# Optimization experiments

Hardware: AMD Instinct MI355X
Metric: run time of the kernel (lower is better)

The kernel has to match this reference:

```python
import jax, jax.numpy as jnp
import numpy as np

B, L, D = 2, 2048, 2048
H, KVH, HD, FD = 8, 1, 256, 64   # heads, kv heads, head_dim, feature_dim
CHUNK = 64


def setup_inputs() -> dict:
    key = jax.random.key(0)
    ks = jax.random.split(key, 8)
    hidden_states = jax.random.normal(ks[0], (B, L, D), dtype=jnp.float32)
    # Gemma-style RoPE tables over half the head dim
    half = HD // 2
    inv_freq = 1.0 / (10000.0 ** (jnp.arange(half, dtype=jnp.float32) / half))
    ang = jnp.arange(L, dtype=jnp.float32)[:, None] * inv_freq[None, :]  # [L, half]
    freqs_cos, freqs_sin = jnp.cos(ang), jnp.sin(ang)
    mask = jnp.ones((1, 1, L, L), dtype=bool)  # unused in linear path
    s = 0.02
    Wq = jax.random.normal(ks[1], (D, H * HD), dtype=jnp.float32) * s
    Wk = jax.random.normal(ks[2], (D, KVH * HD), dtype=jnp.float32) * s
    Wv = jax.random.normal(ks[3], (D, KVH * HD), dtype=jnp.float32) * s
    Wo = jax.random.normal(ks[4], (H * HD, D), dtype=jnp.float32) * s
    fmq = jax.random.normal(ks[5], (H, HD, FD), dtype=jnp.float32) * s
    fmk = jax.random.normal(ks[6], (H, HD, FD), dtype=jnp.float32) * s
    return dict(hidden_states=hidden_states, freqs_cos=freqs_cos, freqs_sin=freqs_sin,
                mask=mask, Wq=Wq, Wk=Wk, Wv=Wv, Wo=Wo, fmq=fmq, fmk=fmk)


def _rope(x, cos, sin):
    # x: [B, L, h, HD]; Gemma complex RoPE: first half = real, second half = imag
    half = x.shape[-1] // 2
    x1, x2 = x[..., :half], x[..., half:]
    c = cos[None, :, None, :]
    s = sin[None, :, None, :]
    return jnp.concatenate([x1 * c - x2 * s, x1 * s + x2 * c], axis=-1)


def _hedgehog(x, W):
    # x: [B, H, L, HD], W: [H, HD, FD] -> softmax over cat([xW, -xW]) -> [B,H,L,2*FD]
    p = jnp.einsum('bhld,hdf->bhlf', x, W)
    return jax.nn.softmax(jnp.concatenate([p, -p], axis=-1), axis=-1)


def _chunk_linear_attn(q, k, v, chunk=CHUNK):
    # q,k: [B,H,L,F]; v: [B,H,L,HD]; chunked causal linear attention
    b, h, l, f = q.shape
    dv = v.shape[-1]
    n = l // chunk
    q = q.reshape(b, h, n, chunk, f) * (f ** -0.5)
    k = k.reshape(b, h, n, chunk, f)
    v = v.reshape(b, h, n, chunk, dv)
    kv = jnp.einsum('bhncf,bhncd->bhnfd', k, v)            # per-chunk KV
    kv = jnp.cumsum(kv, axis=2)
    kv = jnp.concatenate([jnp.zeros_like(kv[:, :, :1]), kv[:, :, :-1]], axis=2)  # exclusive prefix
    inter = jnp.einsum('bhncf,bhnfd->bhncd', q, kv)        # cross-chunk term
    s = jnp.einsum('bhnif,bhnjf->bhnij', q, k)             # intra-chunk scores
    tri = jnp.tril(jnp.ones((chunk, chunk), dtype=bool))
    s = jnp.where(tri, s, 0.0)
    intra = jnp.einsum('bhnij,bhnjd->bhnid', s, v)
    return (inter + intra).reshape(b, h, l, dv)


def reference(hidden_states, freqs_cos, freqs_sin, mask, Wq, Wk, Wv, Wo, fmq, fmk):
    b, l, _ = hidden_states.shape
    q = (hidden_states @ Wq).reshape(b, l, H, HD)
    k = (hidden_states @ Wk).reshape(b, l, KVH, HD)
    v = (hidden_states @ Wv).reshape(b, l, KVH, HD)
    q = _rope(q, freqs_cos, freqs_sin)
    k = _rope(k, freqs_cos, freqs_sin)
    # repeat_interleave kv heads to num_heads (MQA expansion)
    rep = H // KVH
    k = jnp.repeat(k, rep, axis=2)
    v = jnp.repeat(v, rep, axis=2)
    q = jnp.transpose(q, (0, 2, 1, 3))  # [B,H,L,HD]
    k = jnp.transpose(k, (0, 2, 1, 3))
    v = jnp.transpose(v, (0, 2, 1, 3))
    q = _hedgehog(q, fmq)
    k = _hedgehog(k, fmk)
    o = _chunk_linear_attn(q, k, v)                         # [B,H,L,HD]
    o = jnp.transpose(o, (0, 2, 1, 3)).reshape(b, l, H * HD)
    return o @ Wo
```

## Files before the change

### kernel.cpp

```cpp
#include <hip/hip_runtime.h>

#define B_ 2
#define L_ 2048
#define D_ 2048
#define H_ 8
#define HD_ 256
#define FD_ 64
#define F_ 128
#define NC_ 32
#define M_ (B_*L_)
#define SCALE_Q 0.08838834764831845f

typedef unsigned short u16;
typedef __attribute__((ext_vector_type(8))) short bf16x8;
typedef __attribute__((ext_vector_type(8))) unsigned short u16x8;
typedef __attribute__((ext_vector_type(16))) float f32x16;

#define FMA4(a_, s_, v_) { (a_).x += (s_)*(v_).x; (a_).y += (s_)*(v_).y; \
                           (a_).z += (s_)*(v_).z; (a_).w += (s_)*(v_).w; }


__device__ __forceinline__ u16 bf16_rne(float x) {
  unsigned u = __float_as_uint(x);
  return (u16)((u + 0x7fffu + ((u >> 16) & 1u)) >> 16);
}
__device__ __forceinline__ void bf16_split(float x, u16& h, u16& l) {
  unsigned u = __float_as_uint(x);
  unsigned hb = (u + 0x7fffu + ((u >> 16) & 1u)) >> 16;
  h = (u16)hb;
  float hf = __uint_as_float(hb << 16);
  l = bf16_rne(x - hf);
}

__device__ __forceinline__ void gl_lds16(const u16* g, u16* l) {
  __builtin_amdgcn_global_load_lds(
      (const __attribute__((address_space(1))) unsigned int*)g,
      (__attribute__((address_space(3))) unsigned int*)l, 16, 0, 0);
}

__device__ __forceinline__ void wtrans_body(const float* __restrict__ W, int Nsrc,
                                            int n0, u16* __restrict__ dst,
                                            int P, int kt) {
  int t = threadIdx.x;
  int nn = t & 127, kh = t >> 7;
  const float* src = W + (size_t)(kt * 32 + kh * 16) * Nsrc + n0 + nn;
  u16x8 u0, u1;
  #pragma unroll
  for (int kk = 0; kk < 8; ++kk) u0[kk] = bf16_rne(src[(size_t)kk * Nsrc]);
  #pragma unroll
  for (int kk = 0; kk < 8; ++kk) u1[kk] = bf16_rne(src[(size_t)(kk + 8) * Nsrc]);
  size_t base = ((size_t)P * 64 + kt) * 4096 + (size_t)((nn >> 6) & 1) * 2048
              + (size_t)kh * 1024 + (size_t)((nn >> 5) & 1) * 512
              + (size_t)(nn & 31) * 8;
  *(u16x8*)(dst + base) = u0;
  *(u16x8*)(dst + base + 256) = u1;
}

__global__ __launch_bounds__(256)
void prep_kernel(const float* __restrict__ hs,
                 const float* __restrict__ Wq, const float* __restrict__ Wk,
                 const float* __restrict__ Wv,
                 u16* __restrict__ hsHt, u16* __restrict__ hsLt,
                 u16* __restrict__ WTh) {
  int bid = blockIdx.x;
  if (bid < 4096) {
    int gid = bid * 256 + threadIdx.x;
    int r = gid >> 8, u = gid & 255;
    const float* src = hs + (size_t)r * 2048 + u * 8;
    float4 v0 = *(const float4*)src, v1 = *(const float4*)(src + 4);
    float vals[8] = {v0.x, v0.y, v0.z, v0.w, v1.x, v1.y, v1.z, v1.w};
    u16x8 hv, lv;
    #pragma unroll
    for (int j = 0; j < 8; ++j) { u16 hh, ll; bf16_split(vals[j], hh, ll); hv[j] = hh; lv[j] = ll; }
    size_t off = ((size_t)(r >> 6) * 64 + (u >> 2)) * 2048
               + (size_t)((u >> 1) & 1) * 1024 + (size_t)((r >> 5) & 1) * 512
               + (size_t)(u & 1) * 256 + (size_t)(r & 31) * 8;
    *(u16x8*)(hsHt + off) = hv;
    *(u16x8*)(hsLt + off) = lv;
  } else {
    int idx = bid - 4096;
    int P = idx >> 6, kt = idx & 63;
    const float* W; int Nsrc, n0;
    if (P < 16)      { W = Wq; Nsrc = 2048; n0 = P * 128; }
    else if (P < 18) { W = Wk; Nsrc = 256;  n0 = (P - 16) * 128; }
    else             { W = Wv; Nsrc = 256;  n0 = (P - 18) * 128; }
    wtrans_body(W, Nsrc, n0, WTh, P, kt);
  }
}

__global__ __launch_bounds__(256)
void wtrans_wo(const float* __restrict__ Wo, u16* __restrict__ WoTh) {
  wtrans_body(Wo, 2048, blockIdx.x * 128, WoTh, blockIdx.x, blockIdx.y);
}

__device__ __forceinline__ void mfma_body(
    const u16* __restrict__ AtH, const u16* __restrict__ AtL,
    const u16* __restrict__ Bt, float* __restrict__ C, int cstride,
    int bm, int bn) {
  __shared__ __align__(16) u16 AsH[2048];
  __shared__ __align__(16) u16 AsL[2048];
  __shared__ __align__(16) u16 Bs[4096];
  const int t = threadIdx.x, lane = t & 63, wv = t >> 6;
  const u16* aSrc = (wv ? AtL : AtH) + (size_t)bm * 131072 + lane * 8;
  const u16* bSrc = Bt + (size_t)bn * 262144 + wv * 2048 + lane * 8;
  u16* aDst = wv ? AsL : AsH;
  u16* bDst = Bs + wv * 2048;

  f32x16 acc[2][2];
  #pragma unroll
  for (int a = 0; a < 2; ++a)
    #pragma unroll
    for (int b2 = 0; b2 < 2; ++b2)
      #pragma unroll
      for (int r = 0; r < 16; ++r) acc[a][b2][r] = 0.f;

  for (int kt = 0; kt < 64; ++kt) {
    const u16* ak = aSrc + (size_t)kt * 2048;
    const u16* bk = bSrc + (size_t)kt * 4096;
    __syncthreads();
    #pragma unroll
    for (int c = 0; c < 4; ++c) {
      gl_lds16(ak + c * 512, aDst + c * 512);
      gl_lds16(bk + c * 512, bDst + c * 512);
    }
    __syncthreads();

    #pragma unroll
    for (int ks = 0; ks < 2; ++ks) {
      const u16* ph = AsH + ks * 1024 + lane * 8;
      const u16* pl = AsL + ks * 1024 + lane * 8;
      const u16* pb = Bs + wv * 2048 + ks * 1024 + lane * 8;
      bf16x8 a0 = *(const bf16x8*)ph;
      bf16x8 a1 = *(const bf16x8*)(ph + 512);
      bf16x8 b0 = *(const bf16x8*)pb;
      bf16x8 b1 = *(const bf16x8*)(pb + 512);
      acc[0][0] = __builtin_amdgcn_mfma_f32_32x32x16_bf16(a0, b0, acc[0][0], 0, 0, 0);
      acc[0][1] = __builtin_amdgcn_mfma_f32_32x32x16_bf16(a0, b1, acc[0][1], 0, 0, 0);
      acc[1][0] = __builtin_amdgcn_mfma_f32_32x32x16_bf16(a1, b0, acc[1][0], 0, 0, 0);
      acc[1][1] = __builtin_amdgcn_mfma_f32_32x32x16_bf16(a1, b1, acc[1][1], 0, 0, 0);
      bf16x8 l0 = *(const bf16x8*)pl;
      bf16x8 l1 = *(const bf16x8*)(pl + 512);
      acc[0][0] = __builtin_amdgcn_mfma_f32_32x32x16_bf16(l0, b0, acc[0][0], 0, 0, 0);
      acc[0][1] = __builtin_amdgcn_mfma_f32_32x32x16_bf16(l0, b1, acc[0][1], 0, 0, 0);
      acc[1][0] = __builtin_amdgcn_mfma_f32_32x32x16_bf16(l1, b0, acc[1][0], 0, 0, 0);
      acc[1][1] = __builtin_amdgcn_mfma_f32_32x32x16_bf16(l1, b1, acc[1][1], 0, 0, 0);
    }
  }

  const int fr = lane & 31, g = lane >> 5;
  float* Cp = C + (size_t)(bm * 64) * cstride + wv * 64;
  #pragma unroll
  for (int mt = 0; mt < 2; ++mt)
    #pragma unroll
    for (int nt = 0; nt < 2; ++nt) {
      #pragma unroll
      for (int r = 0; r < 16; ++r) {
        int row = mt * 32 + (r & 3) + 8 * (r >> 2) + 4 * g;
        Cp[(size_t)row * cstride + nt * 32 + fr] = acc[mt][nt][r];
      }
    }
}

#define SUB_ 20480

__device__ __forceinline__ void mfma_big_body(
    const u16* __restrict__ AtH, const u16* __restrict__ AtL,
    const u16* __restrict__ Bt, float* __restrict__ C, int cstride,
    int bm, int bn) {
  __shared__ __align__(16) u16 lds[3 * SUB_];
  const int t = threadIdx.x, lane = t & 63, wv = t >> 6;
  const int wm = wv >> 1, wn = wv & 1;

  const u16* gs[5];
  unsigned lo[5], gst[5];
  #pragma unroll
  for (int j = 0; j < 5; ++j) {
    int line = wv * 5 + j;
    if (line < 16) {
      gs[j] = AtH + ((size_t)(4 * bm + (line >> 2)) * 64) * 2048
                  + (size_t)(line & 3) * 512 + lane * 8;
      lo[j] = line * 512; gst[j] = 2048;
    } else if (line < 32) {
      int l2 = line - 16;
      gs[j] = AtL + ((size_t)(4 * bm + (l2 >> 2)) * 64) * 2048
                  + (size_t)(l2 & 3) * 512 + lane * 8;
      lo[j] = 8192 + l2 * 512; gst[j] = 2048;
    } else {
      int l3 = line - 32;
      gs[j] = Bt + (size_t)bn * 262144 + (size_t)l3 * 512 + lane * 8;
      lo[j] = 16384 + l3 * 512; gst[j] = 4096;
    }
  }

  f32x16 acc[2][2];
  #pragma unroll
  for (int a = 0; a < 2; ++a)
    #pragma unroll
    for (int b2 = 0; b2 < 2; ++b2)
      #pragma unroll
      for (int r = 0; r < 16; ++r) acc[a][b2][r] = 0.f;

  auto stage = [&](int kt_, int boff_) {
    #pragma unroll
    for (int j = 0; j < 5; ++j)
      gl_lds16(gs[j] + (size_t)kt_ * gst[j], lds + boff_ + lo[j]);
  };

  stage(0, 0);
  stage(1, SUB_);
  asm volatile("s_waitcnt vmcnt(5)" ::: "memory");
  __builtin_amdgcn_s_barrier();
  __builtin_amdgcn_sched_barrier(0);

  int cb = 0;
  for (int kt = 0; kt < 64; ++kt) {
    int sb = cb + 2 * SUB_; if (sb >= 3 * SUB_) sb -= 3 * SUB_;
    if (kt < 62) stage(kt + 2, sb);
    const u16* base = lds + cb;
    #pragma unroll
    for (int ks = 0; ks < 2; ++ks) {
      const u16* ph = base + wm * 2048 + ks * 1024 + lane * 8;
      const u16* pb = base + 16384 + wn * 2048 + ks * 1024 + lane * 8;
      bf16x8 a0 = *(const bf16x8*)ph;
      bf16x8 a1 = *(const bf16x8*)(ph + 512);
      bf16x8 l0 = *(const bf16x8*)(ph + 8192);
      bf16x8 l1 = *(const bf16x8*)(ph + 8704);
      bf16x8 b0 = *(const bf16x8*)pb;
      bf16x8 b1 = *(const bf16x8*)(pb + 512);
      __builtin_amdgcn_s_setprio(1);
      acc[0][0] = __builtin_amdgcn_mfma_f32_32x32x16_bf16(a0, b0, acc[0][0], 0, 0, 0);
      acc[0][1] = __builtin_amdgcn_mfma_f32_32x32x16_bf16(a0, b1, acc[0][1], 0, 0, 0);
      acc[1][0] = __builtin_amdgcn_mfma_f32_32x32x16_bf16(a1, b0, acc[1][0], 0, 0, 0);
      acc[1][1] = __builtin_amdgcn_mfma_f32_32x32x16_bf16(a1, b1, acc[1][1], 0, 0, 0);
      acc[0][0] = __builtin_amdgcn_mfma_f32_32x32x16_bf16(l0, b0, acc[0][0], 0, 0, 0);
      acc[0][1] = __builtin_amdgcn_mfma_f32_32x32x16_bf16(l0, b1, acc[0][1], 0, 0, 0);
      acc[1][0] = __builtin_amdgcn_mfma_f32_32x32x16_bf16(l1, b0, acc[1][0], 0, 0, 0);
      acc[1][1] = __builtin_amdgcn_mfma_f32_32x32x16_bf16(l1, b1, acc[1][1], 0, 0, 0);
      __builtin_amdgcn_s_setprio(0);
    }
    asm volatile("s_waitcnt lgkmcnt(0)" ::: "memory");
    if (kt < 62) asm volatile("s_waitcnt vmcnt(5)" ::: "memory");
    else         asm volatile("s_waitcnt vmcnt(0)" ::: "memory");
    __builtin_amdgcn_s_barrier();
    __builtin_amdgcn_sched_barrier(0);
    cb += SUB_; if (cb == 3 * SUB_) cb = 0;
  }

  const int fr = lane & 31, g = lane >> 5;
  float* Cp = C + (size_t)(bm * 256 + wm * 64) * cstride + wn * 64;
  #pragma unroll
  for (int mt = 0; mt < 2; ++mt)
    #pragma unroll
    for (int nt = 0; nt < 2; ++nt) {
      #pragma unroll
      for (int r = 0; r < 16; ++r) {
        int row = mt * 32 + (r & 3) + 8 * (r >> 2) + 4 * g;
        Cp[(size_t)row * cstride + nt * 32 + fr] = acc[mt][nt][r];
      }
    }
}

__global__ __launch_bounds__(512, 2)
void mfma_q(const u16* __restrict__ hsHt, const u16* __restrict__ hsLt,
            const u16* __restrict__ WTh, float* __restrict__ q) {
  mfma_big_body(hsHt, hsLt, WTh, q + blockIdx.x * 128, 2048,
                blockIdx.y, blockIdx.x);
}

__global__ __launch_bounds__(128, 4)
void mfma_kv(const u16* __restrict__ hsHt, const u16* __restrict__ hsLt,
             const u16* __restrict__ WTh,
             float* __restrict__ k, float* __restrict__ v) {
  int bn = blockIdx.x;
  float* Cb; int co;
  if (bn < 2) { Cb = k; co = bn * 128; }
  else        { Cb = v; co = (bn - 2) * 128; }
  mfma_body(hsHt, hsLt, WTh, Cb + co, 256, blockIdx.y, 16 + bn);
}

__global__ __launch_bounds__(512, 2)
void mfma_wo(const u16* __restrict__ oHt, const u16* __restrict__ oLt,
             const u16* __restrict__ WoTh, float* __restrict__ out) {
  mfma_big_body(oHt, oLt, WoTh, out + blockIdx.x * 128, 2048,
                blockIdx.y, blockIdx.x);
}

__device__ __forceinline__ float wave_max64(float v) {
  #pragma unroll
  for (int off = 32; off > 0; off >>= 1) v = fmaxf(v, __shfl_xor(v, off, 64));
  return v;
}
__device__ __forceinline__ float wave_sum64(float v) {
  #pragma unroll
  for (int off = 32; off > 0; off >>= 1) v += __shfl_xor(v, off, 64);
  return v;
}

__global__ __launch_bounds__(256)
void hedgehog_kernel(const float* __restrict__ q, const float* __restrict__ kx,
                     const float* __restrict__ fmq, const float* __restrict__ fmk,
                     const float* __restrict__ cosb, const float* __restrict__ sinb,
                     float* __restrict__ qf, float* __restrict__ kf) {
  __shared__ __align__(16) float rows[4][4][256];
  int bid = blockIdx.x;
  const float* x; const float* fm; float* out; int nh_in, gb;
  if (bid < 2048) { x = q;  fm = fmq; out = qf; nh_in = 8; gb = bid * 4; }
  else            { x = kx; fm = fmk; out = kf; nh_in = 1; gb = (bid - 2048) * 4; }
  int wave = threadIdx.x >> 6, lane = threadIdx.x & 63;
  int g = gb + wave;
  int l4 = g & (L_/4 - 1);
  int bh = g / (L_/4);
  int h = bh & 7, b = bh >> 3;
  int l0 = l4 * 4;
  size_t rstride = (nh_in == 1) ? (size_t)HD_ : (size_t)H_ * HD_;
  const float* xrow = (nh_in == 1)
      ? x + (size_t)(b * L_ + l0) * HD_
      : x + ((size_t)(b * L_ + l0) * H_ + h) * HD_;
  int dd = (lane & 31) * 4;
  #pragma unroll
  for (int r = 0; r < 4; ++r) {
    float4 v = *(const float4*)(xrow + r * rstride + lane * 4);
    float4 u;
    u.x = __shfl_xor(v.x, 32, 64); u.y = __shfl_xor(v.y, 32, 64);
    u.z = __shfl_xor(v.z, 32, 64); u.w = __shfl_xor(v.w, 32, 64);
    int l = l0 + r;
    float4 c = *(const float4*)(cosb + (size_t)l * 128 + dd);
    float4 s = *(const float4*)(sinb + (size_t)l * 128 + dd);
    float4 ro;
    if (lane < 32) {
      ro.x = v.x * c.x - u.x * s.x; ro.y = v.y * c.y - u.y * s.y;
      ro.z = v.z * c.z - u.z * s.z; ro.w = v.w * c.w - u.w * s.w;
    } else {
      ro.x = u.x * s.x + v.x * c.x; ro.y = u.y * s.y + v.y * c.y;
      ro.z = u.z * s.z + v.z * c.z; ro.w = u.w * s.w + v.w * c.w;
    }
    *(float4*)&rows[wave][r][lane * 4] = ro;
  }
  __syncthreads();

  const float* fmh = fm + (size_t)h * HD_ * FD_;
  float p0 = 0.f, p1 = 0.f, p2 = 0.f, p3 = 0.f;
  for (int d2 = 0; d2 < HD_; d2 += 4) {
    float w0 = fmh[(d2 + 0) * FD_ + lane];
    float w1 = fmh[(d2 + 1) * FD_ + lane];
    float w2 = fmh[(d2 + 2) * FD_ + lane];
    float w3 = fmh[(d2 + 3) * FD_ + lane];
    float4 r0 = *(const float4*)&rows[wave][0][d2];
    float4 r1 = *(const float4*)&rows[wave][1][d2];
    float4 r2 = *(const float4*)&rows[wave][2][d2];
    float4 r3 = *(const float4*)&rows[wave][3][d2];
    p0 += r0.x * w0 + r0.y * w1 + r0.z * w2 + r0.w * w3;
    p1 += r1.x * w0 + r1.y * w1 + r1.z * w2 + r1.w * w3;
    p2 += r2.x * w0 + r2.y * w1 + r2.z * w2 + r2.w * w3;
    p3 += r3.x * w0 + r3.y * w1 + r3.z * w2 + r3.w * w3;
  }
  float p[4] = {p0, p1, p2, p3};
  #pragma unroll
  for (int r = 0; r < 4; ++r) {
    float m = wave_max64(fabsf(p[r]));
    float e1 = __expf(p[r] - m);
    float e2 = __expf(-p[r] - m);
    float z = wave_sum64(e1 + e2);
    float inv = 1.0f / z;
    size_t base = ((size_t)bh * L_ + l0 + r) * F_;
    out[base + lane]      = e1 * inv;
    out[base + 64 + lane] = e2 * inv;
  }
}

__global__ __launch_bounds__(256)
void chunk_kv_kernel(const float* __restrict__ kf, const float* __restrict__ v,
                     float* __restrict__ kvc) {
  __shared__ __align__(16) float kfs[64][128];
  int n = blockIdx.x & (NC_ - 1), bh = blockIdx.x >> 5;
  int b = bh >> 3;
  const float* kfp = kf + ((size_t)bh * L_ + (size_t)n * 64) * F_;
  int t = threadIdx.x;
  #pragma unroll
  for (int it = 0; it < 8; ++it) {
    int flat = t * 4 + it * 1024;
    *(float4*)&kfs[flat >> 7][flat & 127] = *(const float4*)(kfp + flat);
  }
  __syncthreads();
  int dg = t & 63;
  int fg = t >> 6;
  const float* vp = v + (size_t)(b * L_ + n * 64) * HD_ + dg * 4;
  float* outp = kvc + (size_t)blockIdx.x * (F_ * HD_) + dg * 4;
  #pragma unroll
  for (int pass = 0; pass < 4; ++pass) {
    int f0 = fg * 8 + pass * 32;
    float4 acc[8];
    #pragma unroll
    for (int i = 0; i < 8; ++i) acc[i] = make_float4(0.f, 0.f, 0.f, 0.f);
    for (int j = 0; j < 64; ++j) {
      float4 vv = *(const float4*)(vp + (size_t)j * HD_);
      float4 ka = *(const float4*)&kfs[j][f0];
      float4 kb = *(const float4*)&kfs[j][f0 + 4];
      FMA4(acc[0], ka.x, vv); FMA4(acc[1], ka.y, vv);
      FMA4(acc[2], ka.z, vv); FMA4(acc[3], ka.w, vv);
      FMA4(acc[4], kb.x, vv); FMA4(acc[5], kb.y, vv);
      FMA4(acc[6], kb.z, vv); FMA4(acc[7], kb.w, vv);
    }
    #pragma unroll
    for (int ff = 0; ff < 8; ++ff)
      *(float4*)(outp + (size_t)(f0 + ff) * HD_) = acc[ff];
  }
}

__global__ __launch_bounds__(256)
void chunk_scan_kernel(float* __restrict__ kvc) {
  size_t gid = ((size_t)blockIdx.x * 256 + threadIdx.x) * 4;
  size_t bh = gid >> 15;
  size_t fd = gid & 32767;
  float* p = kvc + bh * ((size_t)NC_ * F_ * HD_) + fd;
  float4 run = make_float4(0.f, 0.f, 0.f, 0.f);
  #pragma unroll
  for (int n = 0; n < NC_; ++n) {
    float4 val = *(float4*)(p + (size_t)n * (F_ * HD_));
    *(float4*)(p + (size_t)n * (F_ * HD_)) = run;
    run.x += val.x; run.y += val.y; run.z += val.z; run.w += val.w;
  }
}

__global__ __launch_bounds__(256)
void chunk_attn_kernel(const float* __restrict__ qf, const float* __restrict__ kf,
                       const float* __restrict__ v, const float* __restrict__ kvc,
                       u16* __restrict__ oHt, u16* __restrict__ oLt) {
  __shared__ __align__(16) float qsT[128][68];
  __shared__ __align__(16) float ksS[128][68];
  float (*ssT)[68] = (float(*)[68])ksS;
  int n = blockIdx.x & (NC_ - 1), bh = blockIdx.x >> 5;
  int h = bh & 7, b = bh >> 3;
  int t = threadIdx.x;
  const float* qp = qf + ((size_t)bh * L_ + (size_t)n * 64) * F_;
  const float* kp = kf + ((size_t)bh * L_ + (size_t)n * 64) * F_;
  #pragma unroll
  for (int it = 0; it < 8; ++it) {
    int flat = t * 4 + it * 1024;
    int j = flat >> 7, f = flat & 127;
    float4 qv = *(const float4*)(qp + flat);
    qsT[f + 0][j] = qv.x * SCALE_Q; qsT[f + 1][j] = qv.y * SCALE_Q;
    qsT[f + 2][j] = qv.z * SCALE_Q; qsT[f + 3][j] = qv.w * SCALE_Q;
    float4 kv_ = *(const float4*)(kp + flat);
    ksS[f + 0][j] = kv_.x; ksS[f + 1][j] = kv_.y;
    ksS[f + 2][j] = kv_.z; ksS[f + 3][j] = kv_.w;
  }
  __syncthreads();

  float4 accs[4];
  {
    int j4 = (t & 15) * 4, i4 = (t >> 4) * 4;
    #pragma unroll
    for (int i = 0; i < 4; ++i) accs[i] = make_float4(0.f, 0.f, 0.f, 0.f);
    for (int f = 0; f < F_; ++f) {
      float4 a4 = *(const float4*)&qsT[f][i4];
      float4 b4 = *(const float4*)&ksS[f][j4];
      FMA4(accs[0], a4.x, b4); FMA4(accs[1], a4.y, b4);
      FMA4(accs[2], a4.z, b4); FMA4(accs[3], a4.w, b4);
    }
  }
  __syncthreads();
  {
    int j4 = (t & 15) * 4, i4 = (t >> 4) * 4;
    #pragma unroll
    for (int ii = 0; ii < 4; ++ii) {
      float sv[4] = {accs[ii].x, accs[ii].y, accs[ii].z, accs[ii].w};
      #pragma unroll
      for (int jj = 0; jj < 4; ++jj) {
        int i = i4 + ii, j = j4 + jj;
        ssT[j][i] = (j <= i) ? sv[jj] : 0.f;
      }
    }
  }
  __syncthreads();

  int dgrp = t & 31, rs = t >> 5;
  int d0 = dgrp * 8;
  int i0 = rs * 8;
  const float* kvp = kvc + (size_t)blockIdx.x * (F_ * HD_) + d0;
  const float* vp = v + (size_t)(b * L_ + n * 64) * HD_ + d0;
  float4 acc[8][2];
  #pragma unroll
  for (int i = 0; i < 8; ++i) {
    acc[i][0] = make_float4(0.f, 0.f, 0.f, 0.f);
    acc[i][1] = make_float4(0.f, 0.f, 0.f, 0.f);
  }
  for (int f = 0; f < F_; ++f) {
    float4 kv0 = *(const float4*)(kvp + (size_t)f * HD_);
    float4 kv1 = *(const float4*)(kvp + (size_t)f * HD_ + 4);
    float4 a0 = *(const float4*)&qsT[f][i0];
    float4 a1 = *(const float4*)&qsT[f][i0 + 4];
    FMA4(acc[0][0], a0.x, kv0); FMA4(acc[0][1], a0.x, kv1);
    FMA4(acc[1][0], a0.y, kv0); FMA4(acc[1][1], a0.y, kv1);
    FMA4(acc[2][0], a0.z, kv0); FMA4(acc[2][1], a0.z, kv1);
    FMA4(acc[3][0], a0.w, kv0); FMA4(acc[3][1], a0.w, kv1);
    FMA4(acc[4][0], a1.x, kv0); FMA4(acc[4][1], a1.x, kv1);
    FMA4(acc[5][0], a1.y, kv0); FMA4(acc[5][1], a1.y, kv1);
    FMA4(acc[6][0], a1.z, kv0); FMA4(acc[6][1], a1.z, kv1);
    FMA4(acc[7][0], a1.w, kv0); FMA4(acc[7][1], a1.w, kv1);
  }
  for (int j = 0; j < 64; ++j) {
    float4 v0 = *(const float4*)(vp + (size_t)j * HD_);
    float4 v1 = *(const float4*)(vp + (size_t)j * HD_ + 4);
    float4 s0 = *(const float4*)&ssT[j][i0];
    float4 s1 = *(const float4*)&ssT[j][i0 + 4];
    FMA4(acc[0][0], s0.x, v0); FMA4(acc[0][1], s0.x, v1);
    FMA4(acc[1][0], s0.y, v0); FMA4(acc[1][1], s0.y, v1);
    FMA4(acc[2][0], s0.z, v0); FMA4(acc[2][1], s0.z, v1);
    FMA4(acc[3][0], s0.w, v0); FMA4(acc[3][1], s0.w, v1);
    FMA4(acc[4][0], s1.x, v0); FMA4(acc[4][1], s1.x, v1);
    FMA4(acc[5][0], s1.y, v0); FMA4(acc[5][1], s1.y, v1);
    FMA4(acc[6][0], s1.z, v0); FMA4(acc[6][1], s1.z, v1);
    FMA4(acc[7][0], s1.w, v0); FMA4(acc[7][1], s1.w, v1);
  }
  int p = (b * L_ + n * 64) >> 6;
  size_t obase = ((size_t)p * 64 + h * 8 + (dgrp >> 2)) * 2048
               + (size_t)((dgrp >> 1) & 1) * 1024 + (size_t)(dgrp & 1) * 256;
  #pragma unroll
  for (int ii = 0; ii < 8; ++ii) {
    int i = i0 + ii;
    size_t off = obase + (size_t)((i >> 5) & 1) * 512 + (size_t)(i & 31) * 8;
    float vals[8] = {acc[ii][0].x, acc[ii][0].y, acc[ii][0].z, acc[ii][0].w,
                     acc[ii][1].x, acc[ii][1].y, acc[ii][1].z, acc[ii][1].w};
    u16x8 hv, lv;
    #pragma unroll
    for (int jj = 0; jj < 8; ++jj) { u16 hh, ll; bf16_split(vals[jj], hh, ll); hv[jj] = hh; lv[jj] = ll; }
    *(u16x8*)(oHt + off) = hv;
    *(u16x8*)(oLt + off) = lv;
  }
}

extern "C" void kernel_launch(void* const* d_in, const int* in_sizes, int n_in,
                              void* d_out, int out_size, void* d_ws, size_t ws_size,
                              hipStream_t stream) {
  const float* hs   = (const float*)d_in[0];
  const float* fcos = (const float*)d_in[1];
  const float* fsin = (const float*)d_in[2];
  const float* Wq  = (const float*)d_in[4];
  const float* Wk  = (const float*)d_in[5];
  const float* Wv  = (const float*)d_in[6];
  const float* Wo  = (const float*)d_in[7];
  const float* fmq = (const float*)d_in[8];
  const float* fmk = (const float*)d_in[9];
  float* out = (float*)d_out;

  float* ws = (float*)d_ws;
  float* q  = ws;
  float* k  = q  + (size_t)M_ * 2048;
  float* v  = k  + (size_t)M_ * 256;
  float* qf = v  + (size_t)M_ * 256;
  float* kf = qf + (size_t)B_ * H_ * L_ * F_;
  float* kv = kf + (size_t)B_ * H_ * L_ * F_;

  u16* hsHt = (u16*)kv;
  u16* hsLt = hsHt + (size_t)M_ * 2048;
  u16* WTh  = hsLt + (size_t)M_ * 2048;
  u16* WoTh = (u16*)kv;
  u16* oHt  = (u16*)q;
  u16* oLt  = oHt + (size_t)M_ * 2048;

  prep_kernel<<<4096 + 1280, 256, 0, stream>>>(hs, Wq, Wk, Wv, hsHt, hsLt, WTh);
  mfma_q<<<dim3(16, 16), 512, 0, stream>>>(hsHt, hsLt, WTh, q);
  mfma_kv<<<dim3(4, 64), 128, 0, stream>>>(hsHt, hsLt, WTh, k, v);
  hedgehog_kernel<<<2048 + 2048, 256, 0, stream>>>(q, k, fmq, fmk, fcos, fsin, qf, kf);
  chunk_kv_kernel<<<B_ * H_ * NC_, 256, 0, stream>>>(kf, v, kv);
  chunk_scan_kernel<<<(B_ * H_ * F_ * HD_) / 1024, 256, 0, stream>>>(kv);
  chunk_attn_kernel<<<B_ * H_ * NC_, 256, 0, stream>>>(qf, kf, v, kv, oHt, oLt);
  wtrans_wo<<<dim3(16, 64), 256, 0, stream>>>(Wo, WoTh);
  mfma_wo<<<dim3(16, 16), 512, 0, stream>>>(oHt, oLt, WoTh, out);
}
```

Before: 538.9 us.

## Move chunk attention onto bf16x3 MFMA with split-bf16 KV state layout

Rewrites the chunked linear-attention kernel to run the intra-chunk scores, masked S·V and Q·KV products on 32x32x16 bf16 MFMA. Each product uses a hi/lo bf16 split (three MFMAs) to keep close to fp32 accuracy. The per-chunk KV state is now stored directly as hi/lo bf16 in an MFMA-friendly tiled layout, and the scan runs on that format. The attention output is written as fp32 and converted by a separate prep_o pass before the output projection. This trades scalar FMA work for matrix-core throughput, at the cost of an extra output pass and repeated split/convert arithmetic.

```diff
diff --git a/kernel.cpp b/kernel.cpp
--- a/kernel.cpp
+++ b/kernel.cpp
@@ -15,6 +15,7 @@
 typedef __attribute__((ext_vector_type(8))) short bf16x8;
 typedef __attribute__((ext_vector_type(8))) unsigned short u16x8;
 typedef __attribute__((ext_vector_type(16))) float f32x16;
+typedef __attribute__((ext_vector_type(4))) unsigned int u32x4;
 
 #define FMA4(a_, s_, v_) { (a_).x += (s_)*(v_).x; (a_).y += (s_)*(v_).y; \
                            (a_).z += (s_)*(v_).z; (a_).w += (s_)*(v_).w; }
@@ -36,6 +37,13 @@
   __builtin_amdgcn_global_load_lds(
       (const __attribute__((address_space(1))) unsigned int*)g,
       (__attribute__((address_space(3))) unsigned int*)l, 16, 0, 0);
+}
+
+__device__ __forceinline__ size_t kvb_off(int d, int f) {
+  return (size_t)(((d >> 7) & 1) * 16384 + ((f >> 5) & 3) * 4096 +
+                  ((d >> 6) & 1) * 2048 + ((f >> 4) & 1) * 1024 +
+                  ((d >> 5) & 1) * 512 + ((f >> 3) & 1) * 256 +
+                  (d & 31) * 8 + (f & 7));
 }
 
 __device__ __forceinline__ void wtrans_body(const float* __restrict__ W, int Nsrc,
@@ -86,6 +94,24 @@
     else             { W = Wv; Nsrc = 256;  n0 = (P - 18) * 128; }
     wtrans_body(W, Nsrc, n0, WTh, P, kt);
   }
+}
+
+__global__ __launch_bounds__(256)
+void prep_o(const float* __restrict__ o, u16* __restrict__ oHt,
+            u16* __restrict__ oLt) {
+  int gid = blockIdx.x * 256 + threadIdx.x;
+  int r = gid >> 8, u = gid & 255;
+  const float* src = o + (size_t)r * 2048 + u * 8;
+  float4 v0 = *(const float4*)src, v1 = *(const float4*)(src + 4);
+  float vals[8] = {v0.x, v0.y, v0.z, v0.w, v1.x, v1.y, v1.z, v1.w};
+  u16x8 hv, lv;
+  #pragma unroll
+  for (int j = 0; j < 8; ++j) { u16 hh, ll; bf16_split(vals[j], hh, ll); hv[j] = hh; lv[j] = ll; }
+  size_t off = ((size_t)(r >> 6) * 64 + (u >> 2)) * 2048
+             + (size_t)((u >> 1) & 1) * 1024 + (size_t)((r >> 5) & 1) * 512
+             + (size_t)(u & 1) * 256 + (size_t)(r & 31) * 8;
+  *(u16x8*)(oHt + off) = hv;
+  *(u16x8*)(oLt + off) = lv;
 }
 
 __global__ __launch_bounds__(256)
@@ -370,7 +396,7 @@
 
 __global__ __launch_bounds__(256)
 void chunk_kv_kernel(const float* __restrict__ kf, const float* __restrict__ v,
-                     float* __restrict__ kvc) {
+                     u16* __restrict__ kvbH, u16* __restrict__ kvbL) {
   __shared__ __align__(16) float kfs[64][128];
   int n = blockIdx.x & (NC_ - 1), bh = blockIdx.x >> 5;
   int b = bh >> 3;
@@ -385,7 +411,7 @@
   int dg = t & 63;
   int fg = t >> 6;
   const float* vp = v + (size_t)(b * L_ + n * 64) * HD_ + dg * 4;
-  float* outp = kvc + (size_t)blockIdx.x * (F_ * HD_) + dg * 4;
+  size_t cb = (size_t)blockIdx.x * 32768;
   #pragma unroll
   for (int pass = 0; pass < 4; ++pass) {
     int f0 = fg * 8 + pass * 32;
@@ -402,132 +428,228 @@
       FMA4(acc[6], kb.z, vv); FMA4(acc[7], kb.w, vv);
     }
     #pragma unroll
-    for (int ff = 0; ff < 8; ++ff)
-      *(float4*)(outp + (size_t)(f0 + ff) * HD_) = acc[ff];
+    for (int c = 0; c < 4; ++c) {
+      u16x8 hv, lv;
+      #pragma unroll
+      for (int ff = 0; ff < 8; ++ff) {
+        float xs = (c == 0) ? acc[ff].x : (c == 1) ? acc[ff].y
+                 : (c == 2) ? acc[ff].z : acc[ff].w;
+        u16 hh, ll; bf16_split(xs, hh, ll); hv[ff] = hh; lv[ff] = ll;
+      }
+      int d = dg * 4 + c;
+      size_t off = cb + kvb_off(d, f0);
+      *(u16x8*)(kvbH + off) = hv;
+      *(u16x8*)(kvbL + off) = lv;
+    }
   }
 }
 
 __global__ __launch_bounds__(256)
-void chunk_scan_kernel(float* __restrict__ kvc) {
-  size_t gid = ((size_t)blockIdx.x * 256 + threadIdx.x) * 4;
-  size_t bh = gid >> 15;
-  size_t fd = gid & 32767;
-  float* p = kvc + bh * ((size_t)NC_ * F_ * HD_) + fd;
-  float4 run = make_float4(0.f, 0.f, 0.f, 0.f);
-  #pragma unroll
+void chunk_scan_kernel(u16* __restrict__ kvbH, u16* __restrict__ kvbL) {
+  int bh = blockIdx.x >> 4, g = blockIdx.x & 15;
+  int d = threadIdx.x;
+  size_t off = kvb_off(d, g * 8);
+  float run[8] = {0.f, 0.f, 0.f, 0.f, 0.f, 0.f, 0.f, 0.f};
   for (int n = 0; n < NC_; ++n) {
-    float4 val = *(float4*)(p + (size_t)n * (F_ * HD_));
-    *(float4*)(p + (size_t)n * (F_ * HD_)) = run;
-    run.x += val.x; run.y += val.y; run.z += val.z; run.w += val.w;
-  }
-}
-
-__global__ __launch_bounds__(256)
+    size_t a = ((size_t)(bh * 32 + n)) * 32768 + off;
+    u16x8 hv = *(u16x8*)(kvbH + a);
+    u16x8 lv = *(u16x8*)(kvbL + a);
+    u16x8 oh, ol;
+    #pragma unroll
+    for (int c = 0; c < 8; ++c) {
+      float val = __uint_as_float((unsigned)hv[c] << 16)
+                + __uint_as_float((unsigned)lv[c] << 16);
+      u16 hh, ll; bf16_split(run[c], hh, ll); oh[c] = hh; ol[c] = ll;
+      run[c] += val;
+    }
+    *(u16x8*)(kvbH + a) = oh;
+    *(u16x8*)(kvbL + a) = ol;
+  }
+}
+
+#define MFB(a_, b_, c_) (c_) = __builtin_amdgcn_mfma_f32_32x32x16_bf16((a_), (b_), (c_), 0, 0, 0)
+
+__global__ __launch_bounds__(256, 2)
 void chunk_attn_kernel(const float* __restrict__ qf, const float* __restrict__ kf,
-                       const float* __restrict__ v, const float* __restrict__ kvc,
-                       u16* __restrict__ oHt, u16* __restrict__ oLt) {
-  __shared__ __align__(16) float qsT[128][68];
-  __shared__ __align__(16) float ksS[128][68];
-  float (*ssT)[68] = (float(*)[68])ksS;
-  int n = blockIdx.x & (NC_ - 1), bh = blockIdx.x >> 5;
-  int h = bh & 7, b = bh >> 3;
-  int t = threadIdx.x;
-  const float* qp = qf + ((size_t)bh * L_ + (size_t)n * 64) * F_;
-  const float* kp = kf + ((size_t)bh * L_ + (size_t)n * 64) * F_;
-  #pragma unroll
-  for (int it = 0; it < 8; ++it) {
-    int flat = t * 4 + it * 1024;
-    int j = flat >> 7, f = flat & 127;
-    float4 qv = *(const float4*)(qp + flat);
-    qsT[f + 0][j] = qv.x * SCALE_Q; qsT[f + 1][j] = qv.y * SCALE_Q;
-    qsT[f + 2][j] = qv.z * SCALE_Q; qsT[f + 3][j] = qv.w * SCALE_Q;
-    float4 kv_ = *(const float4*)(kp + flat);
-    ksS[f + 0][j] = kv_.x; ksS[f + 1][j] = kv_.y;
-    ksS[f + 2][j] = kv_.z; ksS[f + 3][j] = kv_.w;
+                       const float* __restrict__ v,
+                       const u16* __restrict__ kvbH, const u16* __restrict__ kvbL,
+                       float* __restrict__ o) {
+  __shared__ __align__(16) u16 lds[32768];
+  const int n = blockIdx.x & (NC_ - 1), bh = blockIdx.x >> 5;
+  const int h = bh & 7, b = bh >> 3;
+  const int t = threadIdx.x;
+  const int w = t >> 6, i31 = t & 31, G = (t >> 5) & 1;
+  const int l8 = (t & 63) * 8;
+
+  {
+    const float* qp = qf + ((size_t)bh * L_ + (size_t)n * 64) * F_;
+    const float* kp = kf + ((size_t)bh * L_ + (size_t)n * 64) * F_;
+    int o8 = t & 15, ib = t >> 4;
+    #pragma unroll
+    for (int iter = 0; iter < 4; ++iter) {
+      int i = ib + iter * 16;
+      int it = i >> 5, ks = o8 >> 1;
+      int sub = (it * 8 + ks) * 512 + (o8 & 1) * 256 + (i & 31) * 8;
+      {
+        const float* src = qp + (size_t)i * 128 + o8 * 8;
+        float4 a = *(const float4*)src, c = *(const float4*)(src + 4);
+        float vals[8] = {a.x, a.y, a.z, a.w, c.x, c.y, c.z, c.w};
+        u16x8 hv, lv;
+        #pragma unroll
+        for (int j = 0; j < 8; ++j) {
+          u16 hh, ll; bf16_split(vals[j] * SCALE_Q, hh, ll);
+          hv[j] = hh; lv[j] = ll;
+        }
+        *(u16x8*)(lds + sub) = hv;
+        *(u16x8*)(lds + 8192 + sub) = lv;
+      }
+      {
+        const float* src = kp + (size_t)i * 128 + o8 * 8;
+        float4 a = *(const float4*)src, c = *(const float4*)(src + 4);
+        float vals[8] = {a.x, a.y, a.z, a.w, c.x, c.y, c.z, c.w};
+        u16x8 hv, lv;
+        #pragma unroll
+        for (int j = 0; j < 8; ++j) {
+          u16 hh, ll; bf16_split(vals[j], hh, ll);
+          hv[j] = hh; lv[j] = ll;
+        }
+        *(u16x8*)(lds + 16384 + sub) = hv;
+        *(u16x8*)(lds + 24576 + sub) = lv;
+      }
+    }
   }
   __syncthreads();
 
-  float4 accs[4];
+  const u16* Lq  = lds;
+  const u16* Lql = lds + 8192;
+  const u16* Lk  = lds + 16384;
+  const u16* Lkl = lds + 24576;
+
+  f32x16 st[2][2];
+  #pragma unroll
+  for (int a = 0; a < 2; ++a)
+    #pragma unroll
+    for (int c = 0; c < 2; ++c)
+      #pragma unroll
+      for (int r = 0; r < 16; ++r) st[a][c][r] = 0.f;
+
+  #pragma unroll
+  for (int ks = 0; ks < 8; ++ks) {
+    bf16x8 kh0 = *(const bf16x8*)(Lk  + ks * 512 + l8);
+    bf16x8 kh1 = *(const bf16x8*)(Lk  + (8 + ks) * 512 + l8);
+    bf16x8 kl0 = *(const bf16x8*)(Lkl + ks * 512 + l8);
+    bf16x8 kl1 = *(const bf16x8*)(Lkl + (8 + ks) * 512 + l8);
+    bf16x8 qh0 = *(const bf16x8*)(Lq  + ks * 512 + l8);
+    bf16x8 qh1 = *(const bf16x8*)(Lq  + (8 + ks) * 512 + l8);
+    bf16x8 ql0 = *(const bf16x8*)(Lql + ks * 512 + l8);
+    bf16x8 ql1 = *(const bf16x8*)(Lql + (8 + ks) * 512 + l8);
+    MFB(kh0, qh0, st[0][0]); MFB(kh0, ql0, st[0][0]); MFB(kl0, qh0, st[0][0]);
+    MFB(kh0, qh1, st[0][1]); MFB(kh0, ql1, st[0][1]); MFB(kl0, qh1, st[0][1]);
+    MFB(kh1, qh0, st[1][0]); MFB(kh1, ql0, st[1][0]); MFB(kl1, qh0, st[1][0]);
+    MFB(kh1, qh1, st[1][1]); MFB(kh1, ql1, st[1][1]); MFB(kl1, qh1, st[1][1]);
+  }
+
+  bf16x8 sfH[2][4], sfL[2][4];
+  #pragma unroll
+  for (int mt = 0; mt < 2; ++mt) {
+    int iv = mt * 32 + i31;
+    #pragma unroll
+    for (int ksj = 0; ksj < 4; ++ksj) {
+      const int jt = ksj >> 1, kb = ksj & 1;
+      unsigned ph[4], pl[4];
+      #pragma unroll
+      for (int half = 0; half < 2; ++half) {
+        u16 hh[4], ll[4];
+        #pragma unroll
+        for (int c = 0; c < 4; ++c) {
+          int r = 8 * kb + 4 * half + c;
+          int jv = jt * 32 + (r & 3) + 8 * (r >> 2) + 4 * G;
+          float mv = (jv <= iv) ? st[jt][mt][r] : 0.f;
+          u16 h_, l_; bf16_split(mv, h_, l_);
+          hh[c] = h_; ll[c] = l_;
+        }
+        ph[half * 2 + 0] = (unsigned)hh[0] | ((unsigned)hh[1] << 16);
+        ph[half * 2 + 1] = (unsigned)hh[2] | ((unsigned)hh[3] << 16);
+        pl[half * 2 + 0] = (unsigned)ll[0] | ((unsigned)ll[1] << 16);
+        pl[half * 2 + 1] = (unsigned)ll[2] | ((unsigned)ll[3] << 16);
+      }
+      unsigned rH1 = (unsigned)__shfl_xor((int)(G ? ph[0] : ph[2]), 32, 64);
+      unsigned rH2 = (unsigned)__shfl_xor((int)(G ? ph[1] : ph[3]), 32, 64);
+      unsigned rL1 = (unsigned)__shfl_xor((int)(G ? pl[0] : pl[2]), 32, 64);
+      unsigned rL2 = (unsigned)__shfl_xor((int)(G ? pl[1] : pl[3]), 32, 64);
+      u32x4 wH, wL;
+      wH[0] = G ? rH1 : ph[0]; wH[1] = G ? rH2 : ph[1];
+      wH[2] = G ? ph[2] : rH1; wH[3] = G ? ph[3] : rH2;
+      wL[0] = G ? rL1 : pl[0]; wL[1] = G ? rL2 : pl[1];
+      wL[2] = G ? pl[2] : rL1; wL[3] = G ? pl[3] : rL2;
+      sfH[mt][ksj] = __builtin_bit_cast(bf16x8, wH);
+      sfL[mt][ksj] = __builtin_bit_cast(bf16x8, wL);
+    }
+  }
+
+  f32x16 acc[2][2];
+  #pragma unroll
+  for (int a = 0; a < 2; ++a)
+    #pragma unroll
+    for (int c = 0; c < 2; ++c)
+      #pragma unroll
+      for (int r = 0; r < 16; ++r) acc[a][c][r] = 0.f;
+
   {
-    int j4 = (t & 15) * 4, i4 = (t >> 4) * 4;
-    #pragma unroll
-    for (int i = 0; i < 4; ++i) accs[i] = make_float4(0.f, 0.f, 0.f, 0.f);
-    for (int f = 0; f < F_; ++f) {
-      float4 a4 = *(const float4*)&qsT[f][i4];
-      float4 b4 = *(const float4*)&ksS[f][j4];
-      FMA4(accs[0], a4.x, b4); FMA4(accs[1], a4.y, b4);
-      FMA4(accs[2], a4.z, b4); FMA4(accs[3], a4.w, b4);
-    }
-  }
-  __syncthreads();
+    const float* vp = v + (size_t)(b * L_ + n * 64) * HD_;
+    #pragma unroll
+    for (int nt = 0; nt < 2; ++nt) {
+      #pragma unroll
+      for (int ksj = 0; ksj < 4; ++ksj) {
+        const float* vsrc = vp + (size_t)(ksj * 16 + G * 8) * HD_
+                          + w * 64 + nt * 32 + i31;
+        u16x8 vh, vl;
+        #pragma unroll
+        for (int c = 0; c < 8; ++c) {
+          u16 hh, ll; bf16_split(vsrc[(size_t)c * HD_], hh, ll);
+          vh[c] = hh; vl[c] = ll;
+        }
+        bf16x8 vH = __builtin_bit_cast(bf16x8, vh);
+        bf16x8 vL = __builtin_bit_cast(bf16x8, vl);
+        MFB(sfH[0][ksj], vH, acc[0][nt]); MFB(sfL[0][ksj], vH, acc[0][nt]);
+        MFB(sfH[0][ksj], vL, acc[0][nt]);
+        MFB(sfH[1][ksj], vH, acc[1][nt]); MFB(sfL[1][ksj], vH, acc[1][nt]);
+        MFB(sfH[1][ksj], vL, acc[1][nt]);
+      }
+    }
+  }
+
   {
-    int j4 = (t & 15) * 4, i4 = (t >> 4) * 4;
-    #pragma unroll
-    for (int ii = 0; ii < 4; ++ii) {
-      float sv[4] = {accs[ii].x, accs[ii].y, accs[ii].z, accs[ii].w};
-      #pragma unroll
-      for (int jj = 0; jj < 4; ++jj) {
-        int i = i4 + ii, j = j4 + jj;
-        ssT[j][i] = (j <= i) ? sv[jj] : 0.f;
-      }
-    }
-  }
-  __syncthreads();
-
-  int dgrp = t & 31, rs = t >> 5;
-  int d0 = dgrp * 8;
-  int i0 = rs * 8;
-  const float* kvp = kvc + (size_t)blockIdx.x * (F_ * HD_) + d0;
-  const float* vp = v + (size_t)(b * L_ + n * 64) * HD_ + d0;
-  float4 acc[8][2];
-  #pragma unroll
-  for (int i = 0; i < 8; ++i) {
-    acc[i][0] = make_float4(0.f, 0.f, 0.f, 0.f);
-    acc[i][1] = make_float4(0.f, 0.f, 0.f, 0.f);
-  }
-  for (int f = 0; f < F_; ++f) {
-    float4 kv0 = *(const float4*)(kvp + (size_t)f * HD_);
-    float4 kv1 = *(const float4*)(kvp + (size_t)f * HD_ + 4);
-    float4 a0 = *(const float4*)&qsT[f][i0];
-    float4 a1 = *(const float4*)&qsT[f][i0 + 4];
-    FMA4(acc[0][0], a0.x, kv0); FMA4(acc[0][1], a0.x, kv1);
-    FMA4(acc[1][0], a0.y, kv0); FMA4(acc[1][1], a0.y, kv1);
-    FMA4(acc[2][0], a0.z, kv0); FMA4(acc[2][1], a0.z, kv1);
-    FMA4(acc[3][0], a0.w, kv0); FMA4(acc[3][1], a0.w, kv1);
-    FMA4(acc[4][0], a1.x, kv0); FMA4(acc[4][1], a1.x, kv1);
-    FMA4(acc[5][0], a1.y, kv0); FMA4(acc[5][1], a1.y, kv1);
-    FMA4(acc[6][0], a1.z, kv0); FMA4(acc[6][1], a1.z, kv1);
-    FMA4(acc[7][0], a1.w, kv0); FMA4(acc[7][1], a1.w, kv1);
-  }
-  for (int j = 0; j < 64; ++j) {
-    float4 v0 = *(const float4*)(vp + (size_t)j * HD_);
-    float4 v1 = *(const float4*)(vp + (size_t)j * HD_ + 4);
-    float4 s0 = *(const float4*)&ssT[j][i0];
-    float4 s1 = *(const float4*)&ssT[j][i0 + 4];
-    FMA4(acc[0][0], s0.x, v0); FMA4(acc[0][1], s0.x, v1);
-    FMA4(acc[1][0], s0.y, v0); FMA4(acc[1][1], s0.y, v1);
-    FMA4(acc[2][0], s0.z, v0); FMA4(acc[2][1], s0.z, v1);
-    FMA4(acc[3][0], s0.w, v0); FMA4(acc[3][1], s0.w, v1);
-    FMA4(acc[4][0], s1.x, v0); FMA4(acc[4][1], s1.x, v1);
-    FMA4(acc[5][0], s1.y, v0); FMA4(acc[5][1], s1.y, v1);
-    FMA4(acc[6][0], s1.z, v0); FMA4(acc[6][1], s1.z, v1);
-    FMA4(acc[7][0], s1.w, v0); FMA4(acc[7][1], s1.w, v1);
-  }
-  int p = (b * L_ + n * 64) >> 6;
-  size_t obase = ((size_t)p * 64 + h * 8 + (dgrp >> 2)) * 2048
-               + (size_t)((dgrp >> 1) & 1) * 1024 + (size_t)(dgrp & 1) * 256;
-  #pragma unroll
-  for (int ii = 0; ii < 8; ++ii) {
-    int i = i0 + ii;
-    size_t off = obase + (size_t)((i >> 5) & 1) * 512 + (size_t)(i & 31) * 8;
-    float vals[8] = {acc[ii][0].x, acc[ii][0].y, acc[ii][0].z, acc[ii][0].w,
-                     acc[ii][1].x, acc[ii][1].y, acc[ii][1].z, acc[ii][1].w};
-    u16x8 hv, lv;
-    #pragma unroll
-    for (int jj = 0; jj < 8; ++jj) { u16 hh, ll; bf16_split(vals[jj], hh, ll); hv[jj] = hh; lv[jj] = ll; }
-    *(u16x8*)(oHt + off) = hv;
-    *(u16x8*)(oLt + off) = lv;
-  }
+    size_t cb = (size_t)blockIdx.x * 32768;
+    #pragma unroll
+    for (int ks = 0; ks < 8; ++ks) {
+      bf16x8 qa_h0 = *(const bf16x8*)(Lq  + ks * 512 + l8);
+      bf16x8 qa_h1 = *(const bf16x8*)(Lq  + (8 + ks) * 512 + l8);
+      bf16x8 qa_l0 = *(const bf16x8*)(Lql + ks * 512 + l8);
+      bf16x8 qa_l1 = *(const bf16x8*)(Lql + (8 + ks) * 512 + l8);
+      #pragma unroll
+      for (int nt = 0; nt < 2; ++nt) {
+        size_t base = cb + kvb_off(w * 64 + nt * 32, ks * 16) + l8;
+        bf16x8 kvH = *(const bf16x8*)((const short*)(kvbH + base));
+        bf16x8 kvL = *(const bf16x8*)((const short*)(kvbL + base));
+        MFB(qa_h0, kvH, acc[0][nt]); MFB(qa_l0, kvH, acc[0][nt]);
+        MFB(qa_h0, kvL, acc[0][nt]);
+        MFB(qa_h1, kvH, acc[1][nt]); MFB(qa_l1, kvH, acc[1][nt]);
+        MFB(qa_h1, kvL, acc[1][nt]);
+      }
+    }
+  }
+
+  float* op = o + ((size_t)(b * L_ + n * 64)) * 2048 + h * 256 + w * 64;
+  #pragma unroll
+  for (int mt = 0; mt < 2; ++mt)
+    #pragma unroll
+    for (int nt = 0; nt < 2; ++nt)
+      #pragma unroll
+      for (int r = 0; r < 16; ++r) {
+        int row = mt * 32 + (r & 3) + 8 * (r >> 2) + 4 * G;
+        op[(size_t)row * 2048 + nt * 32 + i31] = acc[mt][nt][r];
+      }
 }
 
 extern "C" void kernel_launch(void* const* d_in, const int* in_sizes, int n_in,
@@ -550,22 +672,26 @@
   float* v  = k  + (size_t)M_ * 256;
   float* qf = v  + (size_t)M_ * 256;
   float* kf = qf + (size_t)B_ * H_ * L_ * F_;
-  float* kv = kf + (size_t)B_ * H_ * L_ * F_;
-
-  u16* hsHt = (u16*)kv;
+  float* kvr = kf + (size_t)B_ * H_ * L_ * F_;
+
+  u16* hsHt = (u16*)kvr;
   u16* hsLt = hsHt + (size_t)M_ * 2048;
   u16* WTh  = hsLt + (size_t)M_ * 2048;
-  u16* WoTh = (u16*)kv;
-  u16* oHt  = (u16*)q;
-  u16* oLt  = oHt + (size_t)M_ * 2048;
+  u16* kvbH = (u16*)kvr;
+  u16* kvbL = kvbH + (size_t)512 * 32768;
+  u16* WoTh = (u16*)kvr;
+  float* o  = q;
+  u16* oHt  = (u16*)qf;
+  u16* oLt  = (u16*)kf;
 
   prep_kernel<<<4096 + 1280, 256, 0, stream>>>(hs, Wq, Wk, Wv, hsHt, hsLt, WTh);
   mfma_q<<<dim3(16, 16), 512, 0, stream>>>(hsHt, hsLt, WTh, q);
   mfma_kv<<<dim3(4, 64), 128, 0, stream>>>(hsHt, hsLt, WTh, k, v);
   hedgehog_kernel<<<2048 + 2048, 256, 0, stream>>>(q, k, fmq, fmk, fcos, fsin, qf, kf);
-  chunk_kv_kernel<<<B_ * H_ * NC_, 256, 0, stream>>>(kf, v, kv);
-  chunk_scan_kernel<<<(B_ * H_ * F_ * HD_) / 1024, 256, 0, stream>>>(kv);
-  chunk_attn_kernel<<<B_ * H_ * NC_, 256, 0, stream>>>(qf, kf, v, kv, oHt, oLt);
+  chunk_kv_kernel<<<B_ * H_ * NC_, 256, 0, stream>>>(kf, v, kvbH, kvbL);
+  chunk_scan_kernel<<<256, 256, 0, stream>>>(kvbH, kvbL);
+  chunk_attn_kernel<<<B_ * H_ * NC_, 256, 0, stream>>>(qf, kf, v, kvbH, kvbL, o);
+  prep_o<<<4096, 256, 0, stream>>>(o, oHt, oLt);
   wtrans_wo<<<dim3(16, 64), 256, 0, stream>>>(Wo, WoTh);
   mfma_wo<<<dim3(16, 16), 512, 0, stream>>>(oHt, oLt, WoTh, out);
 }
```

Measured after the change: 558.4 us. +3.6%, slower.
